# Kernel optimization log

Hardware: AMD Instinct MI355X
Metric: run time of the kernel (lower is better)

The kernel has to match this reference:

```python
import jax, jax.numpy as jnp
import numpy as np

B, C, D = 8192, 4, 256
E, H, O = 8, 256, 128
AQ, HQ = 18, 512
THRESH = 0.3
MAX_OUT_REC = 2


def setup_inputs() -> dict:
    key = jax.random.key(0)
    ks = jax.random.split(key, 16)
    s = lambda *sh: 1.0 / np.sqrt(sh[-2] if len(sh) > 1 else sh[-1])
    inp = {
        'data': jax.random.normal(ks[0], (B, C, D), jnp.float32),
        # stacked expert MLPs: D -> H -> O
        'We1': jax.random.normal(ks[1], (E, D, H), jnp.float32) / np.sqrt(D),
        'be1': jnp.zeros((E, H), jnp.float32),
        'We2': jax.random.normal(ks[2], (E, H, O), jnp.float32) / np.sqrt(H),
        'be2': jnp.zeros((E, O), jnp.float32),
        # gating: D -> E (softmax)
        'Wg': jax.random.normal(ks[3], (D, E), jnp.float32) / np.sqrt(D),
        'bg': jnp.zeros((E,), jnp.float32),
        # outer recursive gating: C*O -> 2 (softmax)
        'Wog': jax.random.normal(ks[4], (C * O, 2), jnp.float32) / np.sqrt(C * O),
        'bog': jnp.zeros((2,), jnp.float32),
        # recursive mapping: O -> D
        'Wr': jax.random.normal(ks[5], (O, D), jnp.float32) / np.sqrt(O),
        'br': jnp.zeros((D,), jnp.float32),
        # Q network: C*O -> HQ -> A
        'Wq1': jax.random.normal(ks[6], (C * O, HQ), jnp.float32) / np.sqrt(C * O),
        'bq1': jnp.zeros((HQ,), jnp.float32),
        'Wq2': jax.random.normal(ks[7], (HQ, AQ), jnp.float32) / np.sqrt(HQ),
        'bq2': jnp.zeros((AQ,), jnp.float32),
    }
    return inp


def _moe_forward(x3, We1, be1, We2, be2, Wg, bg):
    # x3: (B, C, D) -> tokens (N, D), N = B*C
    b = x3.shape[0]
    x = x3.reshape(b * C, D)
    # dense all-experts forward
    h = jax.nn.relu(jnp.einsum('nd,edh->enh', x, We1) + be1[:, None, :])  # (E,N,H)
    eo = jnp.einsum('enh,eho->eno', h, We2) + be2[:, None, :]              # (E,N,O)
    g = jax.nn.softmax(x @ Wg + bg, axis=-1)                               # (N,E)
    out = jnp.einsum('ne,eno->no', g, eo)                                  # (N,O)
    return out.reshape(b, C * O)


def reference(data, We1, be1, We2, be2, Wg, bg, Wog, bog, Wr, br, Wq1, bq1, Wq2, bq2):
    result = _moe_forward(data, We1, be1, We2, be2, Wg, bg)               # (B, C*O)
    co = jax.nn.softmax(result @ Wog + bog, axis=-1)                      # (B, 2)
    gate2 = (co[:, 0] > THRESH).astype(result.dtype)[:, None]             # (B, 1)
    # while-loop with per-sample mask; unrolled MAX_OUT_REC iterations is
    # exact: once a sample's mask is 0 its result (hence mask) is unchanged.
    for _ in range(MAX_OUT_REC):
        r_ = result.reshape(data.shape[0] * C, O) @ Wr + br               # recursive_mapping
        r3 = r_.reshape(data.shape[0], C, D)
        out = _moe_forward(r3, We1, be1, We2, be2, Wg, bg)
        result = result + out * co[:, 0:1] * gate2
        co = jax.nn.softmax(result @ Wog + bog, axis=-1)
        gate2 = (co[:, 0] > 0.5).astype(result.dtype)[:, None]
    values = jax.nn.relu(result @ Wq1 + bq1) @ Wq2 + bq2                  # (B, A)
    return values
```

## Files before the change

### kernel.cpp

```cpp
#include <hip/hip_runtime.h>
#include <math.h>


typedef _Float16 f16;
typedef f16   f16x8  __attribute__((ext_vector_type(8)));
typedef f16   f16x4  __attribute__((ext_vector_type(4)));
typedef float f32x16 __attribute__((ext_vector_type(16)));
typedef float v4f    __attribute__((ext_vector_type(4)));

#define MFMA(a, b, c) __builtin_amdgcn_mfma_f32_32x32x16_f16(a, b, c, 0, 0, 0)
#define LO_SCALE 4096.0f
#define LO_INV   (1.0f / 4096.0f)

#define XS 264
#define RS 136
#define QS 520

__device__ __forceinline__ v4f nt_load4(const float* p) {
    return __builtin_nontemporal_load((const v4f*)p);
}
__device__ __forceinline__ f16x8 ldg8(const f16* p) {
    return *(const f16x8*)p;
}

__global__ __launch_bounds__(256) void prep_kernel(
    const float* __restrict__ We1, const float* __restrict__ We2,
    const float* __restrict__ Wr,  const float* __restrict__ Wg,
    const float* __restrict__ Wq1, const float* __restrict__ Wq2,
    f16* __restrict__ W1H, f16* __restrict__ W1L,
    f16* __restrict__ W2H, f16* __restrict__ W2L,
    f16* __restrict__ WrH, f16* __restrict__ WrL,
    f16* __restrict__ WgH, f16* __restrict__ WgL,
    f16* __restrict__ Wq1H, f16* __restrict__ Wq1L,
    f16* __restrict__ Wq2H, f16* __restrict__ Wq2L)
{
    int t = blockIdx.x * 4 + (threadIdx.x >> 6);
    int lane = threadIdx.x & 63;
    const float* src; f16 *dh, *dl;
    int stride, ncols, kbase, nbase, tile;
    if (t < 1024) {
        int e = t >> 7, kt = (t >> 3) & 15, nt = t & 7;
        src = We1 + e * 65536; stride = 256; ncols = 256;
        kbase = kt * 16; nbase = nt * 32; tile = t; dh = W1H; dl = W1L;
    } else if (t < 1536) {
        int i = t - 1024; int e = i >> 6, kt = (i >> 2) & 15, nt = i & 3;
        src = We2 + e * 32768; stride = 128; ncols = 128;
        kbase = kt * 16; nbase = nt * 32; tile = i; dh = W2H; dl = W2L;
    } else if (t < 1600) {
        int i = t - 1536; int kt = i >> 3, nt = i & 7;
        src = Wr; stride = 256; ncols = 256;
        kbase = kt * 16; nbase = nt * 32; tile = i; dh = WrH; dl = WrL;
    } else if (t < 1616) {
        int i = t - 1600;
        src = Wg; stride = 8; ncols = 8;
        kbase = i * 16; nbase = 0; tile = i; dh = WgH; dl = WgL;
    } else if (t < 2128) {
        int i = t - 1616; int kt = i >> 4, nt = i & 15;
        src = Wq1; stride = 512; ncols = 512;
        kbase = kt * 16; nbase = nt * 32; tile = i; dh = Wq1H; dl = Wq1L;
    } else {
        int i = t - 2128;
        src = Wq2; stride = 18; ncols = 18;
        kbase = i * 16; nbase = 0; tile = i; dh = Wq2H; dl = Wq2L;
    }
    int n = lane & 31, kg = lane >> 5;
    int col = nbase + n;
    f16x8 hv, lv;
    #pragma unroll
    for (int j = 0; j < 8; ++j) {
        int k = kbase + kg * 8 + j;
        float w = (col < ncols) ? src[(size_t)k * stride + col] : 0.f;
        f16 h = (f16)w;
        hv[j] = h;
        lv[j] = (f16)((w - (float)h) * LO_SCALE);
    }
    *(f16x8*)(dh + (size_t)tile * 512 + lane * 8) = hv;
    *(f16x8*)(dl + (size_t)tile * 512 + lane * 8) = lv;
}

template<bool REC>
__global__ __launch_bounds__(512, 4) void moe_mfma(
    const float* xsrc, const float* __restrict__ sbuf,
    const f16* __restrict__ W1H, const f16* __restrict__ W1L,
    const f16* __restrict__ W2H, const f16* __restrict__ W2L,
    const f16* __restrict__ WrH, const f16* __restrict__ WrL,
    const f16* __restrict__ WgH, const f16* __restrict__ WgL,
    const float* __restrict__ be1, const float* __restrict__ be2,
    const float* __restrict__ bg,  const float* __restrict__ br,
    float* result)
{
    extern __shared__ char smem[];
    f16* xh = (f16*)smem;
    f16* xl = xh + 32 * XS;
    f16* hh = xl + 32 * XS;
    f16* hl = hh + 32 * XS;

    const int tid = threadIdx.x;
    const int lane = tid & 63;
    const int wv = tid >> 6;
    const int l31 = lane & 31;
    const int kg = lane >> 5;
    const int n0 = blockIdx.x * 32;
    const int nt2 = wv & 3, kh = wv >> 2;

    if (!REC) {
        #pragma unroll
        for (int i = 0; i < 4; ++i) {
            int idx = i * 512 + tid;
            int m = idx >> 6, k4 = (idx & 63) * 4;
            v4f v = nt_load4(&xsrc[(size_t)(n0 + m) * 256 + k4]);
            f16x4 hv, lv;
            #pragma unroll
            for (int j = 0; j < 4; ++j) {
                hv[j] = (f16)v[j];
                lv[j] = (f16)((v[j] - (float)hv[j]) * LO_SCALE);
            }
            *(f16x4*)&xh[m * XS + k4] = hv;
            *(f16x4*)&xl[m * XS + k4] = lv;
        }
    } else {
        f16* rh = hh;
        f16* rl = hl;
        #pragma unroll
        for (int i = 0; i < 2; ++i) {
            int idx = i * 512 + tid;
            int m = idx >> 5, k4 = (idx & 31) * 4;
            v4f v = nt_load4(&xsrc[(size_t)(n0 + m) * 128 + k4]);
            f16x4 hv, lv;
            #pragma unroll
            for (int j = 0; j < 4; ++j) {
                hv[j] = (f16)v[j];
                lv[j] = (f16)((v[j] - (float)hv[j]) * LO_SCALE);
            }
            *(f16x4*)&rh[m * RS + k4] = hv;
            *(f16x4*)&rl[m * RS + k4] = lv;
        }
        __syncthreads();
        f32x16 am = {}, ac = {};
        const f16* wrh = WrH + (size_t)wv * 512 + lane * 8;
        const f16* wrl = WrL + (size_t)wv * 512 + lane * 8;
        #pragma unroll
        for (int kt = 0; kt < 8; ++kt) {
            f16x8 bh = ldg8(wrh + (size_t)kt * 4096);
            f16x8 bl = ldg8(wrl + (size_t)kt * 4096);
            f16x8 ah = *(const f16x8*)&rh[l31 * RS + kt * 16 + kg * 8];
            f16x8 al = *(const f16x8*)&rl[l31 * RS + kt * 16 + kg * 8];
            am = MFMA(ah, bh, am); ac = MFMA(al, bh, ac); ac = MFMA(ah, bl, ac);
        }
        {
            int col = wv * 32 + l31;
            float brv = br[col];
            #pragma unroll
            for (int r = 0; r < 16; ++r) {
                int row = (r & 3) + 8 * (r >> 2) + 4 * kg;
                float v = am[r] + ac[r] * LO_INV + brv;
                f16 hv = (f16)v;
                xh[row * XS + col] = hv;
                xl[row * XS + col] = (f16)((v - (float)hv) * LO_SCALE);
            }
        }
    }
    __syncthreads();

    float gr[16];
    {
        f32x16 gm = {}, gc = {};
        #pragma unroll
        for (int kt = 0; kt < 16; ++kt) {
            f16x8 bh = ldg8(WgH + (size_t)kt * 512 + lane * 8);
            f16x8 bl = ldg8(WgL + (size_t)kt * 512 + lane * 8);
            f16x8 ah = *(const f16x8*)&xh[l31 * XS + kt * 16 + kg * 8];
            f16x8 al = *(const f16x8*)&xl[l31 * XS + kt * 16 + kg * 8];
            gm = MFMA(ah, bh, gm); gc = MFMA(al, bh, gc); gc = MFMA(ah, bl, gc);
        }
        float bge = (l31 < 8) ? bg[l31] : 0.f;
        #pragma unroll
        for (int r = 0; r < 16; ++r) {
            float lg = gm[r] + gc[r] * LO_INV + bge;
            float mx = lg;
            #pragma unroll
            for (int d = 1; d < 8; d <<= 1) mx = fmaxf(mx, __shfl_xor(mx, d, 64));
            float ex = __expf(lg - mx);
            float s = ex;
            #pragma unroll
            for (int d = 1; d < 8; d <<= 1) s += __shfl_xor(s, d, 64);
            gr[r] = ex / s;
        }
    }

    f32x16 out = {};
    #pragma unroll 1
    for (int e = 0; e < 8; ++e) {
        f32x16 am = {}, ac = {};
        const f16* w1h = W1H + (size_t)e * 65536 + (size_t)wv * 512 + lane * 8;
        const f16* w1l = W1L + (size_t)e * 65536 + (size_t)wv * 512 + lane * 8;
        #pragma unroll
        for (int kt = 0; kt < 16; ++kt) {
            f16x8 bh = ldg8(w1h + (size_t)kt * 4096);
            f16x8 bl = ldg8(w1l + (size_t)kt * 4096);
            f16x8 ah = *(const f16x8*)&xh[l31 * XS + kt * 16 + kg * 8];
            f16x8 al = *(const f16x8*)&xl[l31 * XS + kt * 16 + kg * 8];
            am = MFMA(ah, bh, am); ac = MFMA(al, bh, ac); ac = MFMA(ah, bl, ac);
        }
        __syncthreads();
        {
            int col = wv * 32 + l31;
            float b1v = be1[e * 256 + col];
            #pragma unroll
            for (int r = 0; r < 16; ++r) {
                int row = (r & 3) + 8 * (r >> 2) + 4 * kg;
                float v = am[r] + ac[r] * LO_INV + b1v;
                v = fmaxf(v, 0.f);
                f16 hv = (f16)v;
                hh[row * XS + col] = hv;
                hl[row * XS + col] = (f16)((v - (float)hv) * LO_SCALE);
            }
        }
        __syncthreads();
        f32x16 am2 = {}, ac2 = {};
        const f16* w2h = W2H + (size_t)e * 32768 + (size_t)nt2 * 512 + lane * 8;
        const f16* w2l = W2L + (size_t)e * 32768 + (size_t)nt2 * 512 + lane * 8;
        #pragma unroll
        for (int k2 = 0; k2 < 8; ++k2) {
            int kt = kh * 8 + k2;
            f16x8 bh = ldg8(w2h + (size_t)kt * 2048);
            f16x8 bl = ldg8(w2l + (size_t)kt * 2048);
            f16x8 ah = *(const f16x8*)&hh[l31 * XS + kt * 16 + kg * 8];
            f16x8 al = *(const f16x8*)&hl[l31 * XS + kt * 16 + kg * 8];
            am2 = MFMA(ah, bh, am2); ac2 = MFMA(al, bh, ac2); ac2 = MFMA(ah, bl, ac2);
        }
        float be2v = (kh == 0) ? be2[e * 128 + nt2 * 32 + l31] : 0.f;
        #pragma unroll
        for (int r = 0; r < 16; ++r) {
            float eo = am2[r] + ac2[r] * LO_INV + be2v;
            float gv = __shfl(gr[r], (lane & 32) + e, 64);
            out[r] += gv * eo;
        }
    }

    float* red = (float*)hh;
    __syncthreads();
    if (kh == 1) {
        #pragma unroll
        for (int r = 0; r < 16; ++r)
            red[nt2 * 1024 + r * 64 + lane] = out[r];
    }
    __syncthreads();
    if (kh == 0) {
        int col = nt2 * 32 + l31;
        #pragma unroll
        for (int r = 0; r < 16; ++r) {
            int row = (r & 3) + 8 * (r >> 2) + 4 * kg;
            size_t off = (size_t)(n0 + row) * 128 + col;
            float v = out[r] + red[nt2 * 1024 + r * 64 + lane];
            if (REC) {
                float sv = sbuf[(n0 + row) >> 2];
                float old = __builtin_nontemporal_load(&result[off]);
                v = old + v * sv;
            }
            __builtin_nontemporal_store(v, &result[off]);
        }
    }
}

__global__ __launch_bounds__(256) void co_kernel(
    const float* __restrict__ result, const float* __restrict__ Wog,
    const float* __restrict__ bog, float* __restrict__ sbuf, float thresh)
{
    int lane = threadIdx.x & 63;
    int w = threadIdx.x >> 6;
    int b = blockIdx.x * 4 + w;
    const float* r = result + (size_t)b * 512;
    float l0 = 0.f, l1 = 0.f;
    #pragma unroll
    for (int j = 0; j < 8; ++j) {
        int d = j * 64 + lane;
        float rv = __builtin_nontemporal_load(&r[d]);
        float2 wv = *(const float2*)&Wog[d * 2];
        l0 = fmaf(rv, wv.x, l0);
        l1 = fmaf(rv, wv.y, l1);
    }
    #pragma unroll
    for (int off = 32; off > 0; off >>= 1) {
        l0 += __shfl_down(l0, off);
        l1 += __shfl_down(l1, off);
    }
    if (lane == 0) {
        l0 += bog[0]; l1 += bog[1];
        float co0 = 1.f / (1.f + __expf(l1 - l0));
        sbuf[b] = (co0 > thresh) ? co0 : 0.f;
    }
}

__global__ __launch_bounds__(512, 2) void q_mfma(
    const float* __restrict__ result,
    const f16* __restrict__ Wq1H, const f16* __restrict__ Wq1L,
    const f16* __restrict__ Wq2H, const f16* __restrict__ Wq2L,
    const float* __restrict__ bq1, const float* __restrict__ bq2,
    float* __restrict__ out)
{
    extern __shared__ char smem[];
    f16* rh = (f16*)smem;
    f16* rl = rh + 32 * QS;
    f16* hh = rl + 32 * QS;
    f16* hl = hh + 32 * QS;
    float* part = (float*)(hl + 32 * QS);
    const int tid = threadIdx.x;
    const int lane = tid & 63;
    const int wv = tid >> 6;
    const int l31 = lane & 31;
    const int kg = lane >> 5;
    const int n0 = blockIdx.x * 32;

    #pragma unroll
    for (int i = 0; i < 8; ++i) {
        int idx = i * 512 + tid;
        int m = idx >> 7, k4 = (idx & 127) * 4;
        v4f v = nt_load4(&result[(size_t)(n0 + m) * 512 + k4]);
        f16x4 hv, lv;
        #pragma unroll
        for (int j = 0; j < 4; ++j) {
            hv[j] = (f16)v[j];
            lv[j] = (f16)((v[j] - (float)hv[j]) * LO_SCALE);
        }
        *(f16x4*)&rh[m * QS + k4] = hv;
        *(f16x4*)&rl[m * QS + k4] = lv;
    }
    __syncthreads();

    f32x16 am0 = {}, ac0 = {}, am1 = {}, ac1 = {};
    const int nt0 = wv * 2;
    #pragma unroll
    for (int kt = 0; kt < 32; ++kt) {
        f16x8 ah = *(const f16x8*)&rh[l31 * QS + kt * 16 + kg * 8];
        f16x8 al = *(const f16x8*)&rl[l31 * QS + kt * 16 + kg * 8];
        f16x8 b0h = ldg8(Wq1H + (size_t)(kt * 16 + nt0) * 512 + lane * 8);
        f16x8 b0l = ldg8(Wq1L + (size_t)(kt * 16 + nt0) * 512 + lane * 8);
        f16x8 b1h = ldg8(Wq1H + (size_t)(kt * 16 + nt0 + 1) * 512 + lane * 8);
        f16x8 b1l = ldg8(Wq1L + (size_t)(kt * 16 + nt0 + 1) * 512 + lane * 8);
        am0 = MFMA(ah, b0h, am0); ac0 = MFMA(al, b0h, ac0); ac0 = MFMA(ah, b0l, ac0);
        am1 = MFMA(ah, b1h, am1); ac1 = MFMA(al, b1h, ac1); ac1 = MFMA(ah, b1l, ac1);
    }
    #pragma unroll
    for (int t = 0; t < 2; ++t) {
        int col = (nt0 + t) * 32 + l31;
        float b1v = bq1[col];
        #pragma unroll
        for (int r = 0; r < 16; ++r) {
            int row = (r & 3) + 8 * (r >> 2) + 4 * kg;
            float v = (t ? am1[r] + ac1[r] * LO_INV : am0[r] + ac0[r] * LO_INV) + b1v;
            v = fmaxf(v, 0.f);
            f16 hv = (f16)v;
            hh[row * QS + col] = hv;
            hl[row * QS + col] = (f16)((v - (float)hv) * LO_SCALE);
        }
    }
    __syncthreads();

    if (wv < 4) {
        f32x16 am = {}, ac = {};
        #pragma unroll
        for (int k2 = 0; k2 < 8; ++k2) {
            int kt = wv * 8 + k2;
            f16x8 ah = *(const f16x8*)&hh[l31 * QS + kt * 16 + kg * 8];
            f16x8 al = *(const f16x8*)&hl[l31 * QS + kt * 16 + kg * 8];
            f16x8 bh = ldg8(Wq2H + (size_t)kt * 512 + lane * 8);
            f16x8 bl = ldg8(Wq2L + (size_t)kt * 512 + lane * 8);
            am = MFMA(ah, bh, am); ac = MFMA(al, bh, ac); ac = MFMA(ah, bl, ac);
        }
        #pragma unroll
        for (int r = 0; r < 16; ++r) {
            int row = (r & 3) + 8 * (r >> 2) + 4 * kg;
            part[wv * 1024 + row * 32 + l31] = am[r] + ac[r] * LO_INV;
        }
    }
    __syncthreads();
    for (int idx = tid; idx < 1024; idx += 512) {
        int row = idx >> 5, c = idx & 31;
        if (c < 18) {
            float s = part[idx] + part[1024 + idx] + part[2048 + idx] + part[3072 + idx]
                      + bq2[c];
            out[(size_t)(n0 + row) * 18 + c] = s;
        }
    }
}

extern "C" void kernel_launch(void* const* d_in, const int* in_sizes, int n_in,
                              void* d_out, int out_size, void* d_ws, size_t ws_size,
                              hipStream_t stream)
{
    (void)in_sizes; (void)n_in; (void)out_size; (void)ws_size;
    const float* data = (const float*)d_in[0];
    const float* We1  = (const float*)d_in[1];
    const float* be1  = (const float*)d_in[2];
    const float* We2  = (const float*)d_in[3];
    const float* be2  = (const float*)d_in[4];
    const float* Wg   = (const float*)d_in[5];
    const float* bg   = (const float*)d_in[6];
    const float* Wog  = (const float*)d_in[7];
    const float* bog  = (const float*)d_in[8];
    const float* Wr   = (const float*)d_in[9];
    const float* br   = (const float*)d_in[10];
    const float* Wq1  = (const float*)d_in[11];
    const float* bq1  = (const float*)d_in[12];
    const float* Wq2  = (const float*)d_in[13];
    const float* bq2  = (const float*)d_in[14];
    float* outp = (float*)d_out;

    float* result = (float*)d_ws;
    float* sbuf   = result + (size_t)32768 * 128;
    f16* fb = (f16*)((char*)d_ws + 16809984);
    f16* W1H  = fb;
    f16* W1L  = fb + 524288;
    f16* W2H  = fb + 1048576;
    f16* W2L  = fb + 1310720;
    f16* WrH  = fb + 1572864;
    f16* WrL  = fb + 1605632;
    f16* WgH  = fb + 1638400;
    f16* WgL  = fb + 1646592;
    f16* Wq1H = fb + 1654784;
    f16* Wq1L = fb + 1916928;
    f16* Wq2H = fb + 2179072;
    f16* Wq2L = fb + 2195456;

    const int MOE_LDS = 4 * 32 * XS * 2;
    const int Q_LDS   = 4 * 32 * QS * 2 + 4 * 1024 * 4;

    prep_kernel<<<540, 256, 0, stream>>>(We1, We2, Wr, Wg, Wq1, Wq2,
        W1H, W1L, W2H, W2L, WrH, WrL, WgH, WgL, Wq1H, Wq1L, Wq2H, Wq2L);

    moe_mfma<false><<<1024, 512, MOE_LDS, stream>>>(
        data, nullptr, W1H, W1L, W2H, W2L, WrH, WrL, WgH, WgL,
        be1, be2, bg, br, result);
    co_kernel<<<2048, 256, 0, stream>>>(result, Wog, bog, sbuf, 0.3f);
    moe_mfma<true><<<1024, 512, MOE_LDS, stream>>>(
        result, sbuf, W1H, W1L, W2H, W2L, WrH, WrL, WgH, WgL,
        be1, be2, bg, br, result);
    co_kernel<<<2048, 256, 0, stream>>>(result, Wog, bog, sbuf, 0.5f);
    moe_mfma<true><<<1024, 512, MOE_LDS, stream>>>(
        result, sbuf, W1H, W1L, W2H, W2L, WrH, WrL, WgH, WgL,
        be1, be2, bg, br, result);
    q_mfma<<<256, 512, Q_LDS, stream>>>(result, Wq1H, Wq1L, Wq2H, Wq2L,
        bq1, bq2, outp);
}
```

Before: 720.5 us.

## Software-pipeline expert loop: overlap layer-2 of expert e-1 with layer-1 of e

After: 828.8 us. +15.0%, slower.

```diff
diff --git a/kernel.cpp b/kernel.cpp
--- a/kernel.cpp
+++ b/kernel.cpp
@@ -189,11 +189,10 @@
     }
 
     f32x16 out = {};
-    #pragma unroll 1
-    for (int e = 0; e < 8; ++e) {
+    {
         f32x16 am = {}, ac = {};
-        const f16* w1h = W1H + (size_t)e * 65536 + (size_t)wv * 512 + lane * 8;
-        const f16* w1l = W1L + (size_t)e * 65536 + (size_t)wv * 512 + lane * 8;
+        const f16* w1h = W1H + (size_t)wv * 512 + lane * 8;
+        const f16* w1l = W1L + (size_t)wv * 512 + lane * 8;
         #pragma unroll
         for (int kt = 0; kt < 16; ++kt) {
             f16x8 bh = ldg8(w1h + (size_t)kt * 4096);
@@ -202,6 +201,52 @@
             f16x8 al = *(const f16x8*)&xl[l31 * XS + kt * 16 + kg * 8];
             am = MFMA(ah, bh, am); ac = MFMA(al, bh, ac); ac = MFMA(ah, bl, ac);
         }
+        int col = wv * 32 + l31;
+        float b1v = be1[col];
+        #pragma unroll
+        for (int r = 0; r < 16; ++r) {
+            int row = (r & 3) + 8 * (r >> 2) + 4 * kg;
+            float v = fmaxf(am[r] + ac[r] * LO_INV + b1v, 0.f);
+            f16 hv = (f16)v;
+            hh[row * XS + col] = hv;
+            hl[row * XS + col] = (f16)((v - (float)hv) * LO_SCALE);
+        }
+    }
+    __syncthreads();
+
+    #pragma unroll 1
+    for (int e = 1; e < 8; ++e) {
+        f32x16 am = {}, ac = {}, am2 = {}, ac2 = {};
+        const f16* w1h = W1H + (size_t)e * 65536 + (size_t)wv * 512 + lane * 8;
+        const f16* w1l = W1L + (size_t)e * 65536 + (size_t)wv * 512 + lane * 8;
+        const f16* w2h = W2H + (size_t)(e - 1) * 32768 + (size_t)nt2 * 512 + lane * 8;
+        const f16* w2l = W2L + (size_t)(e - 1) * 32768 + (size_t)nt2 * 512 + lane * 8;
+        #pragma unroll
+        for (int kt = 0; kt < 16; ++kt) {
+            f16x8 bh = ldg8(w1h + (size_t)kt * 4096);
+            f16x8 bl = ldg8(w1l + (size_t)kt * 4096);
+            f16x8 ah = *(const f16x8*)&xh[l31 * XS + kt * 16 + kg * 8];
+            f16x8 al = *(const f16x8*)&xl[l31 * XS + kt * 16 + kg * 8];
+            am = MFMA(ah, bh, am); ac = MFMA(al, bh, ac); ac = MFMA(ah, bl, ac);
+            if (kt < 8) {
+                int k2 = kh * 8 + kt;
+                f16x8 b2h = ldg8(w2h + (size_t)k2 * 2048);
+                f16x8 b2l = ldg8(w2l + (size_t)k2 * 2048);
+                f16x8 a2h = *(const f16x8*)&hh[l31 * XS + k2 * 16 + kg * 8];
+                f16x8 a2l = *(const f16x8*)&hl[l31 * XS + k2 * 16 + kg * 8];
+                am2 = MFMA(a2h, b2h, am2);
+                ac2 = MFMA(a2l, b2h, ac2); ac2 = MFMA(a2h, b2l, ac2);
+            }
+        }
+        {
+            float be2v = (kh == 0) ? be2[(e - 1) * 128 + nt2 * 32 + l31] : 0.f;
+            #pragma unroll
+            for (int r = 0; r < 16; ++r) {
+                float eo = am2[r] + ac2[r] * LO_INV + be2v;
+                float gv = __shfl(gr[r], (lane & 32) + (e - 1), 64);
+                out[r] += gv * eo;
+            }
+        }
         __syncthreads();
         {
             int col = wv * 32 + l31;
@@ -209,31 +254,34 @@
             #pragma unroll
             for (int r = 0; r < 16; ++r) {
                 int row = (r & 3) + 8 * (r >> 2) + 4 * kg;
-                float v = am[r] + ac[r] * LO_INV + b1v;
-                v = fmaxf(v, 0.f);
+                float v = fmaxf(am[r] + ac[r] * LO_INV + b1v, 0.f);
                 f16 hv = (f16)v;
                 hh[row * XS + col] = hv;
                 hl[row * XS + col] = (f16)((v - (float)hv) * LO_SCALE);
             }
         }
         __syncthreads();
+    }
+
+    {
         f32x16 am2 = {}, ac2 = {};
-        const f16* w2h = W2H + (size_t)e * 32768 + (size_t)nt2 * 512 + lane * 8;
-        const f16* w2l = W2L + (size_t)e * 32768 + (size_t)nt2 * 512 + lane * 8;
-        #pragma unroll
-        for (int k2 = 0; k2 < 8; ++k2) {
-            int kt = kh * 8 + k2;
-            f16x8 bh = ldg8(w2h + (size_t)kt * 2048);
-            f16x8 bl = ldg8(w2l + (size_t)kt * 2048);
-            f16x8 ah = *(const f16x8*)&hh[l31 * XS + kt * 16 + kg * 8];
-            f16x8 al = *(const f16x8*)&hl[l31 * XS + kt * 16 + kg * 8];
-            am2 = MFMA(ah, bh, am2); ac2 = MFMA(al, bh, ac2); ac2 = MFMA(ah, bl, ac2);
-        }
-        float be2v = (kh == 0) ? be2[e * 128 + nt2 * 32 + l31] : 0.f;
+        const f16* w2h = W2H + (size_t)7 * 32768 + (size_t)nt2 * 512 + lane * 8;
+        const f16* w2l = W2L + (size_t)7 * 32768 + (size_t)nt2 * 512 + lane * 8;
+        #pragma unroll
+        for (int k2l = 0; k2l < 8; ++k2l) {
+            int k2 = kh * 8 + k2l;
+            f16x8 b2h = ldg8(w2h + (size_t)k2 * 2048);
+            f16x8 b2l = ldg8(w2l + (size_t)k2 * 2048);
+            f16x8 a2h = *(const f16x8*)&hh[l31 * XS + k2 * 16 + kg * 8];
+            f16x8 a2l = *(const f16x8*)&hl[l31 * XS + k2 * 16 + kg * 8];
+            am2 = MFMA(a2h, b2h, am2);
+            ac2 = MFMA(a2l, b2h, ac2); ac2 = MFMA(a2h, b2l, ac2);
+        }
+        float be2v = (kh == 0) ? be2[7 * 128 + nt2 * 32 + l31] : 0.f;
         #pragma unroll
         for (int r = 0; r < 16; ++r) {
             float eo = am2[r] + ac2[r] * LO_INV + be2v;
-            float gv = __shfl(gr[r], (lane & 32) + e, 64);
+            float gv = __shfl(gr[r], (lane & 32) + 7, 64);
             out[r] += gv * eo;
         }
     }
```

## Compact active samples and skip gated-off samples in recursive MoE passes

Applied to the files above, without the earlier changes.

New measurement: 896.8 us. +24.5%, slower.

```diff
diff --git a/kernel.cpp b/kernel.cpp
--- a/kernel.cpp
+++ b/kernel.cpp
@@ -81,6 +81,7 @@
 template<bool REC>
 __global__ __launch_bounds__(512, 4) void moe_mfma(
     const float* xsrc, const float* __restrict__ sbuf,
+    const int* __restrict__ nact, const int* __restrict__ alist,
     const f16* __restrict__ W1H, const f16* __restrict__ W1L,
     const f16* __restrict__ W2H, const f16* __restrict__ W2L,
     const f16* __restrict__ WrH, const f16* __restrict__ WrL,
@@ -94,6 +95,7 @@
     f16* xl = xh + 32 * XS;
     f16* hh = xl + 32 * XS;
     f16* hl = hh + 32 * XS;
+    __shared__ int s_idx[8];
 
     const int tid = threadIdx.x;
     const int lane = tid & 63;
@@ -119,13 +121,23 @@
             *(f16x4*)&xl[m * XS + k4] = lv;
         }
     } else {
+        int nA = *nact;
+        if (blockIdx.x * 8 >= nA) return;
+        if (tid < 8) {
+            int s = blockIdx.x * 8 + tid;
+            s_idx[tid] = (s < nA) ? alist[s] : -1;
+        }
+        __syncthreads();
         f16* rh = hh;
         f16* rl = hl;
         #pragma unroll
         for (int i = 0; i < 2; ++i) {
             int idx = i * 512 + tid;
             int m = idx >> 5, k4 = (idx & 31) * 4;
-            v4f v = nt_load4(&xsrc[(size_t)(n0 + m) * 128 + k4]);
+            int sm = s_idx[m >> 2];
+            v4f v = {};
+            if (sm >= 0)
+                v = nt_load4(&xsrc[(size_t)(sm * 4 + (m & 3)) * 128 + k4]);
             f16x4 hv, lv;
             #pragma unroll
             for (int j = 0; j < 4; ++j) {
@@ -251,21 +263,27 @@
         #pragma unroll
         for (int r = 0; r < 16; ++r) {
             int row = (r & 3) + 8 * (r >> 2) + 4 * kg;
-            size_t off = (size_t)(n0 + row) * 128 + col;
             float v = out[r] + red[nt2 * 1024 + r * 64 + lane];
             if (REC) {
-                float sv = sbuf[(n0 + row) >> 2];
-                float old = __builtin_nontemporal_load(&result[off]);
-                v = old + v * sv;
+                int sm = s_idx[row >> 2];
+                if (sm >= 0) {
+                    size_t off = (size_t)(sm * 4 + (row & 3)) * 128 + col;
+                    float sv = sbuf[sm];
+                    float old = __builtin_nontemporal_load(&result[off]);
+                    __builtin_nontemporal_store(old + v * sv, &result[off]);
+                }
+            } else {
+                size_t off = (size_t)(n0 + row) * 128 + col;
+                __builtin_nontemporal_store(v, &result[off]);
             }
-            __builtin_nontemporal_store(v, &result[off]);
         }
     }
 }
 
 __global__ __launch_bounds__(256) void co_kernel(
     const float* __restrict__ result, const float* __restrict__ Wog,
-    const float* __restrict__ bog, float* __restrict__ sbuf, float thresh)
+    const float* __restrict__ bog, float* __restrict__ sbuf, float thresh,
+    int* __restrict__ cnt, int* __restrict__ alist)
 {
     int lane = threadIdx.x & 63;
     int w = threadIdx.x >> 6;
@@ -288,7 +306,12 @@
     if (lane == 0) {
         l0 += bog[0]; l1 += bog[1];
         float co0 = 1.f / (1.f + __expf(l1 - l0));
-        sbuf[b] = (co0 > thresh) ? co0 : 0.f;
+        float s = (co0 > thresh) ? co0 : 0.f;
+        sbuf[b] = s;
+        if (s != 0.f) {
+            int p = atomicAdd(cnt, 1);
+            alist[p] = b;
+        }
     }
 }
 
@@ -422,24 +445,32 @@
     f16* Wq1L = fb + 1916928;
     f16* Wq2H = fb + 2179072;
     f16* Wq2L = fb + 2195456;
+    int* cnt1  = (int*)((char*)d_ws + 21233664);
+    int* cnt2  = cnt1 + 1;
+    int* list1 = cnt1 + 2;
+    int* list2 = list1 + 8192;
 
     const int MOE_LDS = 4 * 32 * XS * 2;
     const int Q_LDS   = 4 * 32 * QS * 2 + 4 * 1024 * 4;
 
+    hipMemsetAsync(cnt1, 0, 8, stream);
+
     prep_kernel<<<540, 256, 0, stream>>>(We1, We2, Wr, Wg, Wq1, Wq2,
         W1H, W1L, W2H, W2L, WrH, WrL, WgH, WgL, Wq1H, Wq1L, Wq2H, Wq2L);
 
     moe_mfma<false><<<1024, 512, MOE_LDS, stream>>>(
-        data, nullptr, W1H, W1L, W2H, W2L, WrH, WrL, WgH, WgL,
-        be1, be2, bg, br, result);
-    co_kernel<<<2048, 256, 0, stream>>>(result, Wog, bog, sbuf, 0.3f);
+        data, nullptr, nullptr, nullptr, W1H, W1L, W2H, W2L, WrH, WrL,
+        WgH, WgL, be1, be2, bg, br, result);
+    co_kernel<<<2048, 256, 0, stream>>>(result, Wog, bog, sbuf, 0.3f,
+        cnt1, list1);
     moe_mfma<true><<<1024, 512, MOE_LDS, stream>>>(
-        result, sbuf, W1H, W1L, W2H, W2L, WrH, WrL, WgH, WgL,
-        be1, be2, bg, br, result);
-    co_kernel<<<2048, 256, 0, stream>>>(result, Wog, bog, sbuf, 0.5f);
+        result, sbuf, cnt1, list1, W1H, W1L, W2H, W2L, WrH, WrL,
+        WgH, WgL, be1, be2, bg, br, result);
+    co_kernel<<<2048, 256, 0, stream>>>(result, Wog, bog, sbuf, 0.5f,
+        cnt2, list2);
     moe_mfma<true><<<1024, 512, MOE_LDS, stream>>>(
-        result, sbuf, W1H, W1L, W2H, W2L, WrH, WrL, WgH, WgL,
-        be1, be2, bg, br, result);
+        result, sbuf, cnt2, list2, W1H, W1L, W2H, W2L, WrH, WrL,
+        WgH, WgL, be1, be2, bg, br, result);
     q_mfma<<<256, 512, Q_LDS, stream>>>(result, Wq1H, Wq1L, Wq2H, Wq2L,
         bq1, bq2, outp);
 }
```
